# Kernel optimization log

Measured on AMD Instinct MI355X. Metric: run time of the kernel, lower is better.

The kernel has to match this reference:

```python
import jax, jax.numpy as jnp
import numpy as np

N_NODES = 100000
N_EDGES = 1600000
IN_CH = 128
HID = 64
N_LAYER = 4
N_CLASS = 10
N_GRAPHS = 512
EPS = 1e-5


def setup_inputs() -> dict:
    key = jax.random.key(0)
    ks = jax.random.split(key, 20)
    x = jax.random.normal(ks[0], (N_NODES, IN_CH), dtype=jnp.float32)
    src = jax.random.randint(ks[1], (N_EDGES,), 0, N_NODES)
    dst = jax.random.randint(ks[2], (N_EDGES,), 0, N_NODES)
    batch = jnp.sort(jax.random.randint(ks[3], (N_NODES,), 0, N_GRAPHS))
    s = 0.05
    W0 = jax.random.normal(ks[4], (IN_CH, HID), dtype=jnp.float32) * s
    Ws = jax.random.normal(ks[5], (N_LAYER - 1, HID, HID), dtype=jnp.float32) * s
    bs = jax.random.normal(ks[6], (N_LAYER, HID), dtype=jnp.float32) * s
    g_bn = jnp.ones((N_LAYER, HID), dtype=jnp.float32)
    b_bn = jnp.zeros((N_LAYER, HID), dtype=jnp.float32)
    m3 = 3 * N_LAYER * HID  # 768
    m2 = 2 * N_LAYER * HID  # 512
    m1 = N_LAYER * HID      # 256
    g_out = jnp.ones((m3,), dtype=jnp.float32)
    b_out = jnp.zeros((m3,), dtype=jnp.float32)
    w1 = jax.random.normal(ks[7], (m3, m2), dtype=jnp.float32) * s
    b1 = jnp.zeros((m2,), dtype=jnp.float32)
    w2 = jax.random.normal(ks[8], (m2, m1), dtype=jnp.float32) * s
    b2 = jnp.zeros((m1,), dtype=jnp.float32)
    w3 = jax.random.normal(ks[9], (m1, N_CLASS), dtype=jnp.float32) * s
    b3 = jnp.zeros((N_CLASS,), dtype=jnp.float32)
    return dict(x=x, src=src, dst=dst, batch=batch, W0=W0, Ws=Ws, bs=bs,
                g_bn=g_bn, b_bn=b_bn, g_out=g_out, b_out=b_out,
                w1=w1, b1=b1, w2=w2, b2=b2, w3=w3, b3=b3)


def _bn(h, g, b):
    # training-mode BatchNorm1d over rows (biased variance, as torch normalizes)
    m = jnp.mean(h, axis=0)
    v = jnp.var(h, axis=0)
    return (h - m) * jax.lax.rsqrt(v + EPS) * g + b


def reference(x, src, dst, batch, W0, Ws, bs, g_bn, b_bn, g_out, b_out,
              w1, b1, w2, b2, w3, b3):
    n = x.shape[0]
    loops = jnp.arange(n)
    s = jnp.concatenate([src, loops])  # self-loops (GCNConv)
    d = jnp.concatenate([dst, loops])
    deg = jax.ops.segment_sum(jnp.ones_like(s, dtype=x.dtype), d, num_segments=n)
    norm = jax.lax.rsqrt(jnp.maximum(deg, 1.0))
    coef = (norm[s] * norm[d])[:, None]

    def conv(h, W, bias):
        h = h @ W
        msg = h[s] * coef  # [E+N, HID] gather
        return jax.ops.segment_sum(msg, d, num_segments=n) + bias

    H = []
    h = conv(x, W0, bs[0])           # conv_act is identity (default)
    h = _bn(h, g_bn[0], b_bn[0])
    H.append(h)
    for i in range(N_LAYER - 1):
        h = conv(h, Ws[i], bs[i + 1])
        h = _bn(h, g_bn[i + 1], b_bn[i + 1])
        H.append(h)
    H = jnp.concatenate(H, axis=1)   # [N, n_layer*HID]

    # mean / add / max pooling by graph id
    add = jax.ops.segment_sum(H, batch, num_segments=N_GRAPHS)
    cnt = jax.ops.segment_sum(jnp.ones((n,), H.dtype), batch, num_segments=N_GRAPHS)
    avg = add / jnp.maximum(cnt, 1.0)[:, None]
    mx = jax.ops.segment_max(H, batch, num_segments=N_GRAPHS)
    mx = jnp.where(cnt[:, None] > 0, mx, 0.0)
    Hg = jnp.concatenate([avg, add, mx], axis=1)  # [G, 3*n_layer*HID]

    # funnel readout (dropout p=0 -> identity)
    z = _bn(Hg, g_out, b_out)
    z = jax.nn.relu(z @ w1 + b1)
    z = jax.nn.relu(z @ w2 + b2)
    return jax.nn.log_softmax(z @ w3 + b3, axis=1)
```

## Files before the change

### kernel.cpp

```cpp
#include <hip/hip_runtime.h>
#include <hip/hip_bf16.h>
#include <math.h>

#define HIDC 64
#define NLAYER 4
#define NG 512
#define M3 768
#define M2 512
#define M1 256
#define NCLS 10
#define EPSV 1e-5f
#define NB 512
#define EPT 16
#define NPW 2
#define NSH 16

typedef float f32x4 __attribute__((ext_vector_type(4)));
typedef short sh8   __attribute__((ext_vector_type(8)));

__device__ inline unsigned bf16rne(float x){
  unsigned u = __float_as_uint(x);
  return (u + 0x7fffu + ((u >> 16) & 1u)) >> 16;
}
__device__ inline unsigned packbf2(float lo, float hi){
  return bf16rne(lo) | (bf16rne(hi) << 16);
}
__device__ inline float blo(unsigned u){ return __uint_as_float(u << 16); }
__device__ inline float bhi(unsigned u){ return __uint_as_float(u & 0xffff0000u); }

__device__ inline sh8 ldfrag(const unsigned short* p){
  union { uint4 u; sh8 s; } c;
  c.u = *(const uint4*)p;
  return c.s;
}

__global__ __launch_bounds__(256) void k_bhist(const int* __restrict__ dst, int E,
                                               int* __restrict__ bcnt){
  __shared__ int lc[NB];
  int tid = threadIdx.x;
  for (int i = tid; i < NB; i += 256) lc[i] = 0;
  __syncthreads();
  for (int e = blockIdx.x*256 + tid; e < E; e += gridDim.x*256)
    atomicAdd(&lc[__builtin_nontemporal_load(&dst[e]) >> 8], 1);
  __syncthreads();
  for (int i = tid; i < NB; i += 256){
    int c = lc[i];
    if (c) atomicAdd(&bcnt[i], c);
  }
}

__global__ void k_bscan(const int* __restrict__ bcnt, int* __restrict__ bofs,
                        int* __restrict__ bcursor){
  __shared__ int tmp[NB];
  int tid = threadIdx.x;
  int v = bcnt[tid];
  tmp[tid] = v; __syncthreads();
  for (int ofs = 1; ofs < NB; ofs <<= 1){
    int t = (tid >= ofs) ? tmp[tid-ofs] : 0;
    __syncthreads();
    tmp[tid] += t;
    __syncthreads();
  }
  int ex = tmp[tid] - v;
  bofs[tid] = ex;
  bcursor[tid] = ex;
}

__global__ __launch_bounds__(256) void k_bscatter(const int* __restrict__ src,
    const int* __restrict__ dst, int E, int* __restrict__ bcursor, unsigned* __restrict__ stage){
  __shared__ int lcnt[NB];
  __shared__ int lbase[NB];
  int tid = threadIdx.x;
  int t0 = blockIdx.x*(256*EPT);
  for (int i = tid; i < NB; i += 256) lcnt[i] = 0;
  __syncthreads();
  int s_[EPT], d_[EPT];
  bool ok[EPT];
  #pragma unroll
  for (int i = 0; i < EPT; i++){
    int e = t0 + i*256 + tid;
    ok[i] = (e < E);
    int ee = ok[i] ? e : 0;
    d_[i] = __builtin_nontemporal_load(&dst[ee]);
    s_[i] = __builtin_nontemporal_load(&src[ee]);
    if (ok[i]) atomicAdd(&lcnt[d_[i] >> 8], 1);
  }
  __syncthreads();
  for (int i = tid; i < NB; i += 256){
    int c = lcnt[i];
    lbase[i] = c ? atomicAdd(&bcursor[i], c) : 0;
  }
  __syncthreads();
  #pragma unroll
  for (int i = 0; i < EPT; i++){
    if (ok[i]){
      int pos = atomicAdd(&lbase[d_[i] >> 8], 1);
      stage[pos] = ((unsigned)s_[i] << 8) | ((unsigned)d_[i] & 255u);
    }
  }
}

__global__ __launch_bounds__(256) void k_deg_b(const unsigned* __restrict__ stage,
    const int* __restrict__ bofs, const int* __restrict__ bcnt,
    int* __restrict__ row_start, int* __restrict__ cursor,
    float* __restrict__ normv, int n, int E){
  __shared__ int hist[256];
  __shared__ int tmp[256];
  int b = blockIdx.x;
  int tid = threadIdx.x;
  hist[tid] = 0;
  __syncthreads();
  int st = bofs[b], en = st + bcnt[b];
  for (int i = st + tid; i < en; i += 256)
    atomicAdd(&hist[stage[i] & 255u], 1);
  __syncthreads();
  int v = hist[tid];
  tmp[tid] = v;
  __syncthreads();
  for (int o = 1; o < 256; o <<= 1){
    int t = (tid >= o) ? tmp[tid-o] : 0;
    __syncthreads();
    tmp[tid] += t;
    __syncthreads();
  }
  int node = b*256 + tid;
  if (node < n){
    int rs = st + tmp[tid] - v;
    row_start[node] = rs;
    cursor[node] = rs;
    normv[node] = rsqrtf((float)(v + 1));
  }
  if (b == 0 && tid == 0) row_start[n] = E;
}

__global__ __launch_bounds__(256) void k_fill_b(const unsigned* __restrict__ stage,
    const int* __restrict__ bofs, const int* __restrict__ bcnt,
    int* __restrict__ cursor, int* __restrict__ col){
  int b = blockIdx.x;
  int st = bofs[b], en = st + bcnt[b];
  for (int i = st + threadIdx.x; i < en; i += 256){
    unsigned p = stage[i];
    int node = (b << 8) | (int)(p & 255u);
    int pos = atomicAdd(&cursor[node], 1);
    col[pos] = (int)(p >> 8);
  }
}

__global__ __launch_bounds__(256) void k_prep0(const float* __restrict__ W,
    unsigned short* __restrict__ Wt){
  int tid = threadIdx.x;
  int c = tid & 63, q = tid >> 6;
  #pragma unroll 4
  for (int k = q*32; k < q*32 + 32; k++){
    float w = W[(size_t)k*64 + c];
    Wt[(size_t)c*128 + k] = (unsigned short)bf16rne(w);
  }
}

__global__ __launch_bounds__(256) void k_prep_bn(const float* __restrict__ sums,
    const float* __restrict__ g, const float* __restrict__ b, float invn,
    float* __restrict__ bnss_l, const float* __restrict__ W,
    unsigned short* __restrict__ Wt, float* __restrict__ bvec){
  __shared__ float ss[128];
  __shared__ float bred[4][64];
  int tid = threadIdx.x;
  if (tid < 64){
    float s1 = 0.f, s2 = 0.f;
    #pragma unroll
    for (int s = 0; s < NSH; s++){ s1 += sums[s*128 + tid]; s2 += sums[s*128 + 64 + tid]; }
    float mean = s1*invn;
    float var = fmaxf(s2*invn - mean*mean, 0.f);
    float sv = g[tid]*rsqrtf(var + EPSV);
    float sh = b[tid] - mean*sv;
    ss[tid] = sv; ss[64+tid] = sh;
    bnss_l[tid] = sv; bnss_l[64+tid] = sh;
  }
  __syncthreads();
  if (!W) return;
  int c = tid & 63, q = tid >> 6;
  float bs = 0.f;
  #pragma unroll 4
  for (int k = q*16; k < q*16 + 16; k++){
    float w = W[(size_t)k*64 + c];
    Wt[(size_t)c*64 + k] = (unsigned short)bf16rne(w*ss[k]);
    bs += ss[64+k]*w;
  }
  bred[q][c] = bs;
  __syncthreads();
  if (tid < 64) bvec[tid] = bred[0][tid]+bred[1][tid]+bred[2][tid]+bred[3][tid];
}

__device__ inline void mfma_epi(f32x4 acc[2][4], int rowbase, int lr, int lk,
    const float* __restrict__ norm, const float* __restrict__ bias,
    unsigned short* __restrict__ Ub, int n){
  #pragma unroll
  for (int m = 0; m < 2; m++){
    #pragma unroll
    for (int j = 0; j < 4; j++){
      int row = rowbase + m*16 + lk*4 + j;
      if (row < n){
        float nr = norm[row];
        #pragma unroll
        for (int ct = 0; ct < 4; ct++){
          int colv = ct*16 + lr;
          float v = acc[m][ct][j];
          if (bias) v += bias[colv];
          Ub[(size_t)row*64 + colv] = (unsigned short)bf16rne(v*nr);
        }
      }
    }
  }
}

__global__ __launch_bounds__(256) void k_gemm_l0_mfma(const float* __restrict__ X,
    const unsigned short* __restrict__ Wt, const float* __restrict__ norm,
    unsigned* __restrict__ U32, int n){
  __shared__ unsigned short Al[128*40];
  int tid = threadIdx.x;
  int w = tid >> 6, l = tid & 63;
  int lr = l & 15, lk = l >> 4;
  int rb = blockIdx.x * 128;
  f32x4 z = {0.f,0.f,0.f,0.f};
  f32x4 acc[2][4];
  #pragma unroll
  for (int m = 0; m < 2; m++)
    #pragma unroll
    for (int ct = 0; ct < 4; ct++) acc[m][ct] = z;
  for (int kc = 0; kc < 128; kc += 32){
    __syncthreads();
    {
      int r = tid >> 1, h = tid & 1;
      int rr = rb + r; if (rr >= n) rr = n - 1;
      const float* xp = X + (size_t)rr*128 + kc + h*16;
      float4 v0 = *(const float4*)(xp+0);
      float4 v1 = *(const float4*)(xp+4);
      float4 v2 = *(const float4*)(xp+8);
      float4 v3 = *(const float4*)(xp+12);
      uint4 o0, o1;
      o0.x = packbf2(v0.x, v0.y); o0.y = packbf2(v0.z, v0.w);
      o0.z = packbf2(v1.x, v1.y); o0.w = packbf2(v1.z, v1.w);
      o1.x = packbf2(v2.x, v2.y); o1.y = packbf2(v2.z, v2.w);
      o1.z = packbf2(v3.x, v3.y); o1.w = packbf2(v3.z, v3.w);
      unsigned short* dl = &Al[r*40 + h*16];
      *(uint4*)(dl) = o0;
      *(uint4*)(dl+8) = o1;
    }
    __syncthreads();
    sh8 bfr[4];
    #pragma unroll
    for (int ct = 0; ct < 4; ct++)
      bfr[ct] = ldfrag(&Wt[(size_t)(ct*16+lr)*128 + kc + lk*8]);
    #pragma unroll
    for (int m = 0; m < 2; m++){
      sh8 af = ldfrag(&Al[(w*32 + m*16 + lr)*40 + lk*8]);
      #pragma unroll
      for (int ct = 0; ct < 4; ct++)
        acc[m][ct] = __builtin_amdgcn_mfma_f32_16x16x32_bf16(af, bfr[ct], acc[m][ct], 0, 0, 0);
    }
  }
  mfma_epi(acc, rb + w*32, lr, lk, norm, nullptr, (unsigned short*)U32, n);
}

__global__ __launch_bounds__(256) void k_gemm_lb_mfma(const unsigned short* __restrict__ Ab,
    const unsigned short* __restrict__ Wt, const float* __restrict__ bias,
    const float* __restrict__ norm, unsigned* __restrict__ U32, int n){
  int tid = threadIdx.x;
  int w = tid >> 6, l = tid & 63;
  int lr = l & 15, lk = l >> 4;
  int rb = blockIdx.x * 128 + w*32;
  f32x4 z = {0.f,0.f,0.f,0.f};
  f32x4 acc[2][4];
  #pragma unroll
  for (int m = 0; m < 2; m++)
    #pragma unroll
    for (int ct = 0; ct < 4; ct++) acc[m][ct] = z;
  #pragma unroll
  for (int kc = 0; kc < 64; kc += 32){
    sh8 bfr[4];
    #pragma unroll
    for (int ct = 0; ct < 4; ct++)
      bfr[ct] = ldfrag(&Wt[(size_t)(ct*16+lr)*64 + kc + lk*8]);
    #pragma unroll
    for (int m = 0; m < 2; m++){
      int r = rb + m*16 + lr; if (r >= n) r = n - 1;
      sh8 af = ldfrag(&Ab[(size_t)r*64 + kc + lk*8]);
      #pragma unroll
      for (int ct = 0; ct < 4; ct++)
        acc[m][ct] = __builtin_amdgcn_mfma_f32_16x16x32_bf16(af, bfr[ct], acc[m][ct], 0, 0, 0);
    }
  }
  mfma_epi(acc, rb, lr, lk, norm, bias, (unsigned short*)U32, n);
}

__global__ __launch_bounds__(256) void k_agg_bn(const unsigned* __restrict__ U32,
    const int* __restrict__ row_start, const int* __restrict__ col,
    const float* __restrict__ norm, unsigned* __restrict__ AGGb,
    float* __restrict__ sums, int n){
  int tid = threadIdx.x;
  int wv = tid >> 6;
  int lane = tid & 63;
  int half = lane >> 5;
  int cl = lane & 31;
  float rs0=0.f, rs1=0.f, rq0=0.f, rq1=0.f;
  int base = blockIdx.x*(4*NPW) + wv*NPW;
  #pragma unroll
  for (int it = 0; it < NPW; ++it){
    int node = __builtin_amdgcn_readfirstlane(base + it);
    bool nv = (node < n);
    int nodec = nv ? node : 0;
    int st = row_start[nodec], en = row_start[nodec+1];
    float s0 = 0.f, s1 = 0.f;
    if (half == 0){
      unsigned u = U32[(size_t)nodec*32 + cl];
      s0 = blo(u); s1 = bhi(u);
    }
    int nit = (en - st + 15) >> 4;
    for (int i = 0; i < nit; i++){
      int k = st + i*16 + half*8;
      unsigned ua[8];
      #pragma unroll
      for (int j = 0; j < 8; j++){
        int kk = k + j;
        bool v = (kk < en);
        int idx = v ? kk : st;
        unsigned a = U32[(size_t)col[idx]*32 + cl];
        ua[j] = v ? a : 0u;
      }
      #pragma unroll
      for (int j = 0; j < 8; j++){
        s0 += blo(ua[j]);
        s1 += bhi(ua[j]);
      }
    }
    s0 += __shfl_xor(s0, 32);
    s1 += __shfl_xor(s1, 32);
    if (half == 0 && nv){
      float nr = norm[node];
      s0 *= nr; s1 *= nr;
      AGGb[(size_t)node*32 + cl] = packbf2(s0, s1);
      rs0 += s0; rs1 += s1; rq0 += s0*s0; rq1 += s1*s1;
    }
  }
  __shared__ float L[4][32][4];
  if (half == 0){ L[wv][cl][0]=rs0; L[wv][cl][1]=rs1; L[wv][cl][2]=rq0; L[wv][cl][3]=rq1; }
  __syncthreads();
  if (tid < 128){
    int c2 = tid & 31, f = tid >> 5;
    float v = L[0][c2][f] + L[1][c2][f] + L[2][c2][f] + L[3][c2][f];
    int addr = ((f >= 2) ? 64 : 0) + 2*c2 + (f & 1);
    atomicAdd(&sums[(blockIdx.x & (NSH-1))*128 + addr], v);
  }
}

__device__ inline int lowerb(const int* a, int n, int key){
  int lo = 0, hi = n;
  while (lo < hi){ int mid = (lo+hi) >> 1; if (a[mid] < key) lo = mid+1; else hi = mid; }
  return lo;
}

__global__ __launch_bounds__(256) void k_pool_part(const unsigned* __restrict__ AGGall,
    size_t lstride32, const float* __restrict__ bnss, const int* __restrict__ batch,
    int n, float* __restrict__ Ppart){
  int bid = blockIdx.x;
  int g = bid >> 3, sub = bid & 7;
  int c = threadIdx.x;
  int l = c >> 6, ch = c & 63;
  const unsigned* A = AGGall + (size_t)l * lstride32;
  float sc = bnss[l*128 + ch], sh = bnss[l*128 + 64 + ch];
  int hi16 = ch & 1;
  int uofs = ch >> 1;
  int st = lowerb(batch, n, g), en = lowerb(batch, n, g+1);
  int len = en - st;
  int r0 = st + (int)(((long long)sub * len) >> 3);
  int r1 = st + (int)(((long long)(sub+1) * len) >> 3);
  float s = 0.f, mx = -INFINITY;
  for (int r = r0; r < r1; r++){
    unsigned u = A[(size_t)r*32 + uofs];
    float v = hi16 ? bhi(u) : blo(u);
    v = v*sc + sh;
    s += v; mx = fmaxf(mx, v);
  }
  float* P = Ppart + (size_t)bid*512;
  P[c] = s;
  P[256 + c] = mx;
}

__global__ __launch_bounds__(256) void k_pool_comb(const float* __restrict__ Ppart,
    const int* __restrict__ batch, int n, float* __restrict__ Hg){
  int g = blockIdx.x; int c = threadIdx.x;
  float s = 0.f, mx = -INFINITY;
  #pragma unroll
  for (int sub = 0; sub < 8; sub++){
    const float* P = Ppart + (size_t)(g*8 + sub)*512;
    s += P[c];
    mx = fmaxf(mx, P[256 + c]);
  }
  int st = lowerb(batch, n, g), en = lowerb(batch, n, g+1);
  int cnt = en - st;
  float avg = s / (float)(cnt > 1 ? cnt : 1);
  float mo = (cnt > 0) ? mx : 0.f;
  Hg[(size_t)g*M3 + c]        = avg;
  Hg[(size_t)g*M3 + 256 + c]  = s;
  Hg[(size_t)g*M3 + 512 + c]  = mo;
}

__global__ void k_bn2(const float* __restrict__ Hg, const float* __restrict__ g,
                      const float* __restrict__ b, float* __restrict__ zsc, float* __restrict__ zsh){
  int c = blockIdx.x; int tid = threadIdx.x;
  float s1 = 0.f, s2 = 0.f;
  for (int r = tid; r < NG; r += 64){
    float v = Hg[(size_t)r*M3 + c];
    s1 += v; s2 += v*v;
  }
  for (int o = 32; o > 0; o >>= 1){ s1 += __shfl_down(s1, o); s2 += __shfl_down(s2, o); }
  if (tid == 0){
    float mean = s1/(float)NG;
    float var = s2/(float)NG - mean*mean;
    var = fmaxf(var, 0.f);
    float sc = g[c]*rsqrtf(var + EPSV);
    zsc[c] = sc;
    zsh[c] = b[c] - mean*sc;
  }
}

__global__ __launch_bounds__(256) void k_gemm_t(const float* __restrict__ A, int K,
    const float* __restrict__ W, int N, const float* __restrict__ bias,
    const float* __restrict__ zsc, const float* __restrict__ zsh,
    float* __restrict__ out, int relu, int applybn){
  __shared__ float As[32][36];
  __shared__ float Bs[32][36];
  int tid = threadIdx.x;
  int tx = tid & 15, ty = tid >> 4;
  int rb = blockIdx.y << 5, cb = blockIdx.x << 5;
  int lr = tid >> 3;
  int lk = (tid & 7) << 2;
  float acc00=0.f, acc01=0.f, acc10=0.f, acc11=0.f;
  for (int k0 = 0; k0 < K; k0 += 32){
    float4 av = *(const float4*)&A[(size_t)(rb+lr)*K + k0 + lk];
    if (applybn){
      av.x = av.x*zsc[k0+lk+0] + zsh[k0+lk+0];
      av.y = av.y*zsc[k0+lk+1] + zsh[k0+lk+1];
      av.z = av.z*zsc[k0+lk+2] + zsh[k0+lk+2];
      av.w = av.w*zsc[k0+lk+3] + zsh[k0+lk+3];
    }
    *(float4*)&As[lr][lk] = av;
    float4 bv = *(const float4*)&W[(size_t)(k0+lr)*N + cb + lk];
    Bs[lk+0][lr] = bv.x;
    Bs[lk+1][lr] = bv.y;
    Bs[lk+2][lr] = bv.z;
    Bs[lk+3][lr] = bv.w;
    __syncthreads();
    #pragma unroll
    for (int kk = 0; kk < 32; kk += 4){
      float4 a0 = *(const float4*)&As[ty][kk];
      float4 a1 = *(const float4*)&As[ty+16][kk];
      float4 b0 = *(const float4*)&Bs[tx][kk];
      float4 b1 = *(const float4*)&Bs[tx+16][kk];
      acc00 += a0.x*b0.x + a0.y*b0.y + a0.z*b0.z + a0.w*b0.w;
      acc01 += a0.x*b1.x + a0.y*b1.y + a0.z*b1.z + a0.w*b1.w;
      acc10 += a1.x*b0.x + a1.y*b0.y + a1.z*b0.z + a1.w*b0.w;
      acc11 += a1.x*b1.x + a1.y*b1.y + a1.z*b1.z + a1.w*b1.w;
    }
    __syncthreads();
  }
  int c0 = cb + tx, c1 = cb + tx + 16;
  float bz0 = bias[c0], bz1 = bias[c1];
  acc00 += bz0; acc01 += bz1; acc10 += bz0; acc11 += bz1;
  if (relu){
    acc00 = fmaxf(acc00, 0.f); acc01 = fmaxf(acc01, 0.f);
    acc10 = fmaxf(acc10, 0.f); acc11 = fmaxf(acc11, 0.f);
  }
  out[(size_t)(rb+ty)*N + c0]      = acc00;
  out[(size_t)(rb+ty)*N + c1]      = acc01;
  out[(size_t)(rb+ty+16)*N + c0]   = acc10;
  out[(size_t)(rb+ty+16)*N + c1]   = acc11;
}

__global__ __launch_bounds__(256) void k_gemm3_lsm(const float* __restrict__ A,
    const float* __restrict__ W, const float* __restrict__ bias, float* __restrict__ out){
  __shared__ float Wl[M1*NCLS];
  __shared__ float part[64][4][NCLS];
  int tid = threadIdx.x;
  for (int i = tid; i < M1*NCLS; i += 256) Wl[i] = W[i];
  __syncthreads();
  int r = blockIdx.x*64 + (tid >> 2);
  int q = tid & 3;
  float acc[NCLS];
  #pragma unroll
  for (int j = 0; j < NCLS; j++) acc[j] = 0.f;
  const float4* A4 = (const float4*)(A + (size_t)r*M1 + q*64);
  for (int kq = 0; kq < 16; kq++){
    float4 a = A4[kq];
    int kb = q*64 + kq*4;
    #pragma unroll
    for (int j = 0; j < NCLS; j++){
      acc[j] += a.x*Wl[(kb+0)*NCLS+j] + a.y*Wl[(kb+1)*NCLS+j]
              + a.z*Wl[(kb+2)*NCLS+j] + a.w*Wl[(kb+3)*NCLS+j];
    }
  }
  #pragma unroll
  for (int j = 0; j < NCLS; j++) part[tid>>2][q][j] = acc[j];
  __syncthreads();
  if (tid < 64){
    int rr = blockIdx.x*64 + tid;
    float v[NCLS]; float m = -INFINITY;
    #pragma unroll
    for (int j = 0; j < NCLS; j++){
      v[j] = part[tid][0][j] + part[tid][1][j] + part[tid][2][j] + part[tid][3][j] + bias[j];
      m = fmaxf(m, v[j]);
    }
    float s = 0.f;
    #pragma unroll
    for (int j = 0; j < NCLS; j++) s += expf(v[j] - m);
    float ls = logf(s) + m;
    #pragma unroll
    for (int j = 0; j < NCLS; j++) out[(size_t)rr*NCLS + j] = v[j] - ls;
  }
}

extern "C" void kernel_launch(void* const* d_in, const int* in_sizes, int n_in,
                              void* d_out, int out_size, void* d_ws, size_t ws_size,
                              hipStream_t stream){
  const float* x    = (const float*)d_in[0];
  const int*   src  = (const int*)d_in[1];
  const int*   dst  = (const int*)d_in[2];
  const int*   batch= (const int*)d_in[3];
  const float* W0   = (const float*)d_in[4];
  const float* Wsm  = (const float*)d_in[5];
  const float* g_bn = (const float*)d_in[7];
  const float* b_bn = (const float*)d_in[8];
  const float* g_out= (const float*)d_in[9];
  const float* b_out= (const float*)d_in[10];
  const float* w1   = (const float*)d_in[11];
  const float* b1   = (const float*)d_in[12];
  const float* w2   = (const float*)d_in[13];
  const float* b2   = (const float*)d_in[14];
  const float* w3   = (const float*)d_in[15];
  const float* b3   = (const float*)d_in[16];

  int n = in_sizes[3];
  int E = in_sizes[1];

  char* ws = (char*)d_ws;
  size_t off = 0;
  auto alloc = [&](size_t bytes) -> char* {
    char* p = ws + off;
    off += (bytes + 255) / 256 * 256;
    return p;
  };
  float* normv     = (float*)alloc((size_t)n*4);
  int*   row_start = (int*)  alloc((size_t)(n+1)*4);
  int*   cursor    = (int*)  alloc((size_t)n*4);
  int*   colA      = (int*)  alloc((size_t)E*4);
  int*   bcnt      = (int*)  alloc(NB*4);
  int*   bofs      = (int*)  alloc(NB*4);
  int*   bcursor   = (int*)  alloc(NB*4);
  unsigned* stage  = (unsigned*)alloc((size_t)E*4);
  unsigned* U32    = (unsigned*)alloc((size_t)n*32*4);
  size_t lstride32 = (size_t)n*32;
  unsigned* AGGall = (unsigned*)alloc((size_t)NLAYER*lstride32*4);
  float* bnsums    = (float*)alloc(NSH*128*4);
  float* bnss      = (float*)alloc(NLAYER*128*4);
  unsigned short* Wt = (unsigned short*)alloc((size_t)NLAYER*64*128*2);
  float* bvec      = (float*)alloc(NLAYER*64*4);
  float* Ppart     = (float*)alloc((size_t)NG*8*512*4);
  float* Hg        = (float*)alloc((size_t)NG*M3*4);
  float* Z1        = (float*)alloc((size_t)NG*M2*4);
  float* Z2        = (float*)alloc((size_t)NG*M1*4);
  float* zsc       = (float*)alloc(M3*4);
  float* zsh       = (float*)alloc(M3*4);

  int nb_used = (n + 255) >> 8;
  int gb128 = (n + 127) / 128;

  hipMemsetAsync(bcnt, 0, NB*4, stream);
  k_prep0<<<1, 256, 0, stream>>>(W0, Wt);
  k_bhist<<<512, 256, 0, stream>>>(dst, E, bcnt);
  k_bscan<<<1, NB, 0, stream>>>(bcnt, bofs, bcursor);
  { int tiles = (E + 256*EPT - 1)/(256*EPT);
    k_bscatter<<<tiles, 256, 0, stream>>>(src, dst, E, bcursor, stage); }
  k_deg_b<<<nb_used, 256, 0, stream>>>(stage, bofs, bcnt, row_start, cursor, normv, n, E);
  k_fill_b<<<nb_used, 256, 0, stream>>>(stage, bofs, bcnt, cursor, colA);

  float invn = 1.f / (float)n;
  int aggblocks = (n + 4*NPW - 1) / (4*NPW);
  for (int l = 0; l < NLAYER; l++){
    unsigned* AGGb = AGGall + (size_t)l*lstride32;
    if (l == 0)
      k_gemm_l0_mfma<<<gb128, 256, 0, stream>>>(x, Wt, normv, U32, n);
    else
      k_gemm_lb_mfma<<<gb128, 256, 0, stream>>>((const unsigned short*)(AGGall + (size_t)(l-1)*lstride32),
                                                Wt + (size_t)l*64*128, bvec + l*64,
                                                normv, U32, n);
    hipMemsetAsync(bnsums, 0, NSH*128*4, stream);
    k_agg_bn<<<aggblocks, 256, 0, stream>>>(U32, row_start, colA, normv, AGGb, bnsums, n);
    if (l + 1 < NLAYER)
      k_prep_bn<<<1, 256, 0, stream>>>(bnsums, g_bn + l*64, b_bn + l*64, invn,
                                       bnss + l*128, Wsm + (size_t)l*64*64,
                                       Wt + (size_t)(l+1)*64*128, bvec + (l+1)*64);
    else
      k_prep_bn<<<1, 256, 0, stream>>>(bnsums, g_bn + l*64, b_bn + l*64, invn,
                                       bnss + l*128, nullptr, nullptr, nullptr);
  }

  k_pool_part<<<NG*8, 256, 0, stream>>>(AGGall, lstride32, bnss, batch, n, Ppart);
  k_pool_comb<<<NG, 256, 0, stream>>>(Ppart, batch, n, Hg);
  k_bn2<<<M3, 64, 0, stream>>>(Hg, g_out, b_out, zsc, zsh);

  { dim3 g1(M2/32, NG/32); k_gemm_t<<<g1, 256, 0, stream>>>(Hg, M3, w1, M2, b1, zsc, zsh, Z1, 1, 1); }
  { dim3 g2(M1/32, NG/32); k_gemm_t<<<g2, 256, 0, stream>>>(Z1, M2, w2, M1, b2, nullptr, nullptr, Z2, 1, 0); }
  k_gemm3_lsm<<<NG/64, 256, 0, stream>>>(Z2, w3, b3, (float*)d_out);
}
```

Baseline: 439.0 us.

## Pad CSR rows to multiples of 16 with dummy zero node, widen gather lanes

Each node's adjacency row is padded to a multiple of 16 entries, and the padding points at an extra all-zero row of U32. This lets the aggregation loop drop per-edge bounds checks. The aggregation kernel now has 16 lanes per feature group, each loading 8 bytes (4 bf16 channels), with four neighbor groups per wave, and combines them with two shuffle stages. Building the padded CSR takes extra kernels (partial-block scan, row fixup, col prefill), and the padding adds wasted gather work on low-degree nodes.

New measurement: 458.2 us. +4.4%, slower.

```diff
diff --git a/kernel.cpp b/kernel.cpp
--- a/kernel.cpp
+++ b/kernel.cpp
@@ -102,8 +102,8 @@
 
 __global__ __launch_bounds__(256) void k_deg_b(const unsigned* __restrict__ stage,
     const int* __restrict__ bofs, const int* __restrict__ bcnt,
-    int* __restrict__ row_start, int* __restrict__ cursor,
-    float* __restrict__ normv, int n, int E){
+    int* __restrict__ row_start, int* __restrict__ pbsum,
+    float* __restrict__ normv, int n){
   __shared__ int hist[256];
   __shared__ int tmp[256];
   int b = blockIdx.x;
@@ -115,7 +115,8 @@
     atomicAdd(&hist[stage[i] & 255u], 1);
   __syncthreads();
   int v = hist[tid];
-  tmp[tid] = v;
+  int pd = (v + 15) & ~15;
+  tmp[tid] = pd;
   __syncthreads();
   for (int o = 1; o < 256; o <<= 1){
     int t = (tid >= o) ? tmp[tid-o] : 0;
@@ -125,12 +126,41 @@
   }
   int node = b*256 + tid;
   if (node < n){
-    int rs = st + tmp[tid] - v;
-    row_start[node] = rs;
-    cursor[node] = rs;
+    row_start[node] = tmp[tid] - pd;
     normv[node] = rsqrtf((float)(v + 1));
   }
-  if (b == 0 && tid == 0) row_start[n] = E;
+  if (tid == 255) pbsum[b] = tmp[255];
+}
+
+__global__ void k_pbscan(const int* __restrict__ pbsum, int* __restrict__ pbofs,
+                         int* __restrict__ row_start, int n){
+  __shared__ int tmp[NB];
+  int tid = threadIdx.x;
+  int v = pbsum[tid];
+  tmp[tid] = v; __syncthreads();
+  for (int ofs = 1; ofs < NB; ofs <<= 1){
+    int t = (tid >= ofs) ? tmp[tid-ofs] : 0;
+    __syncthreads();
+    tmp[tid] += t;
+    __syncthreads();
+  }
+  pbofs[tid] = tmp[tid] - v;
+  if (tid == NB-1) row_start[n] = tmp[NB-1];
+}
+
+__global__ void k_rowfix(int* __restrict__ row_start, const int* __restrict__ pbofs,
+                         int* __restrict__ cursor, int n){
+  int i = blockIdx.x*256 + threadIdx.x;
+  if (i < n){
+    int r = row_start[i] + pbofs[i >> 8];
+    row_start[i] = r;
+    cursor[i] = r;
+  }
+}
+
+__global__ void k_prefill(int* __restrict__ col, int PE, int n){
+  int i = blockIdx.x*256 + threadIdx.x;
+  if (i < PE) col[i] = n;
 }
 
 __global__ __launch_bounds__(256) void k_fill_b(const unsigned* __restrict__ stage,
@@ -296,12 +326,15 @@
     const int* __restrict__ row_start, const int* __restrict__ col,
     const float* __restrict__ norm, unsigned* __restrict__ AGGb,
     float* __restrict__ sums, int n){
+  const char* Ubase = (const char*)U32;
   int tid = threadIdx.x;
   int wv = tid >> 6;
   int lane = tid & 63;
-  int half = lane >> 5;
-  int cl = lane & 31;
-  float rs0=0.f, rs1=0.f, rq0=0.f, rq1=0.f;
+  int g = lane >> 4;
+  int cl4 = lane & 15;
+  unsigned cofs = (unsigned)(cl4 << 3);
+  float rs[4] = {0.f,0.f,0.f,0.f};
+  float rq[4] = {0.f,0.f,0.f,0.f};
   int base = blockIdx.x*(4*NPW) + wv*NPW;
   #pragma unroll
   for (int it = 0; it < NPW; ++it){
@@ -309,45 +342,51 @@
     bool nv = (node < n);
     int nodec = nv ? node : 0;
     int st = row_start[nodec], en = row_start[nodec+1];
-    float s0 = 0.f, s1 = 0.f;
-    if (half == 0){
-      unsigned u = U32[(size_t)nodec*32 + cl];
-      s0 = blo(u); s1 = bhi(u);
-    }
-    int nit = (en - st + 15) >> 4;
+    uint2 su = *(const uint2*)(Ubase + ((size_t)nodec << 7) + cofs);
+    float s0 = (g==0) ? blo(su.x) : 0.f;
+    float s1 = (g==0) ? bhi(su.x) : 0.f;
+    float s2 = (g==0) ? blo(su.y) : 0.f;
+    float s3 = (g==0) ? bhi(su.y) : 0.f;
+    int nit = (en - st) >> 4;
     for (int i = 0; i < nit; i++){
-      int k = st + i*16 + half*8;
-      unsigned ua[8];
-      #pragma unroll
-      for (int j = 0; j < 8; j++){
-        int kk = k + j;
-        bool v = (kk < en);
-        int idx = v ? kk : st;
-        unsigned a = U32[(size_t)col[idx]*32 + cl];
-        ua[j] = v ? a : 0u;
-      }
-      #pragma unroll
-      for (int j = 0; j < 8; j++){
-        s0 += blo(ua[j]);
-        s1 += bhi(ua[j]);
-      }
-    }
-    s0 += __shfl_xor(s0, 32);
-    s1 += __shfl_xor(s1, 32);
-    if (half == 0 && nv){
+      int k = st + i*16 + g;
+      int j0 = col[k];
+      int j1 = col[k+4];
+      int j2 = col[k+8];
+      int j3 = col[k+12];
+      uint2 a0 = *(const uint2*)(Ubase + ((size_t)j0 << 7) + cofs);
+      uint2 a1 = *(const uint2*)(Ubase + ((size_t)j1 << 7) + cofs);
+      uint2 a2 = *(const uint2*)(Ubase + ((size_t)j2 << 7) + cofs);
+      uint2 a3 = *(const uint2*)(Ubase + ((size_t)j3 << 7) + cofs);
+      s0 += blo(a0.x) + blo(a1.x) + blo(a2.x) + blo(a3.x);
+      s1 += bhi(a0.x) + bhi(a1.x) + bhi(a2.x) + bhi(a3.x);
+      s2 += blo(a0.y) + blo(a1.y) + blo(a2.y) + blo(a3.y);
+      s3 += bhi(a0.y) + bhi(a1.y) + bhi(a2.y) + bhi(a3.y);
+    }
+    s0 += __shfl_xor(s0, 16); s1 += __shfl_xor(s1, 16);
+    s2 += __shfl_xor(s2, 16); s3 += __shfl_xor(s3, 16);
+    s0 += __shfl_xor(s0, 32); s1 += __shfl_xor(s1, 32);
+    s2 += __shfl_xor(s2, 32); s3 += __shfl_xor(s3, 32);
+    if (g == 0 && nv){
       float nr = norm[node];
-      s0 *= nr; s1 *= nr;
-      AGGb[(size_t)node*32 + cl] = packbf2(s0, s1);
-      rs0 += s0; rs1 += s1; rq0 += s0*s0; rq1 += s1*s1;
-    }
-  }
-  __shared__ float L[4][32][4];
-  if (half == 0){ L[wv][cl][0]=rs0; L[wv][cl][1]=rs1; L[wv][cl][2]=rq0; L[wv][cl][3]=rq1; }
+      s0 *= nr; s1 *= nr; s2 *= nr; s3 *= nr;
+      uint2 o; o.x = packbf2(s0, s1); o.y = packbf2(s2, s3);
+      *(uint2*)&AGGb[(size_t)node*32 + cl4*2] = o;
+      rs[0] += s0; rs[1] += s1; rs[2] += s2; rs[3] += s3;
+      rq[0] += s0*s0; rq[1] += s1*s1; rq[2] += s2*s2; rq[3] += s3*s3;
+    }
+  }
+  __shared__ float L[4][16][8];
+  if (g == 0){
+    #pragma unroll
+    for (int q = 0; q < 4; q++){ L[wv][cl4][q] = rs[q]; L[wv][cl4][4+q] = rq[q]; }
+  }
   __syncthreads();
   if (tid < 128){
-    int c2 = tid & 31, f = tid >> 5;
-    float v = L[0][c2][f] + L[1][c2][f] + L[2][c2][f] + L[3][c2][f];
-    int addr = ((f >= 2) ? 64 : 0) + 2*c2 + (f & 1);
+    int c4 = tid >> 3, slot = tid & 7;
+    float v = L[0][c4][slot] + L[1][c4][slot] + L[2][c4][slot] + L[3][c4][slot];
+    int ch = c4*4 + (slot & 3);
+    int addr = ((slot >= 4) ? 64 : 0) + ch;
     atomicAdd(&sums[(blockIdx.x & (NSH-1))*128 + addr], v);
   }
 }
@@ -548,15 +587,18 @@
     off += (bytes + 255) / 256 * 256;
     return p;
   };
+  int PE = E + 16*n;
   float* normv     = (float*)alloc((size_t)n*4);
   int*   row_start = (int*)  alloc((size_t)(n+1)*4);
   int*   cursor    = (int*)  alloc((size_t)n*4);
-  int*   colA      = (int*)  alloc((size_t)E*4);
+  int*   colA      = (int*)  alloc((size_t)PE*4);
   int*   bcnt      = (int*)  alloc(NB*4);
   int*   bofs      = (int*)  alloc(NB*4);
   int*   bcursor   = (int*)  alloc(NB*4);
+  int*   pbsum     = (int*)  alloc(NB*4);
+  int*   pbofs     = (int*)  alloc(NB*4);
   unsigned* stage  = (unsigned*)alloc((size_t)E*4);
-  unsigned* U32    = (unsigned*)alloc((size_t)n*32*4);
+  unsigned* U32    = (unsigned*)alloc((size_t)(n+1)*32*4);
   size_t lstride32 = (size_t)n*32;
   unsigned* AGGall = (unsigned*)alloc((size_t)NLAYER*lstride32*4);
   float* bnsums    = (float*)alloc(NSH*128*4);
@@ -574,12 +616,17 @@
   int gb128 = (n + 127) / 128;
 
   hipMemsetAsync(bcnt, 0, NB*4, stream);
+  hipMemsetAsync(pbsum, 0, NB*4, stream);
+  hipMemsetAsync(U32 + (size_t)n*32, 0, 128, stream);
   k_prep0<<<1, 256, 0, stream>>>(W0, Wt);
   k_bhist<<<512, 256, 0, stream>>>(dst, E, bcnt);
   k_bscan<<<1, NB, 0, stream>>>(bcnt, bofs, bcursor);
   { int tiles = (E + 256*EPT - 1)/(256*EPT);
     k_bscatter<<<tiles, 256, 0, stream>>>(src, dst, E, bcursor, stage); }
-  k_deg_b<<<nb_used, 256, 0, stream>>>(stage, bofs, bcnt, row_start, cursor, normv, n, E);
+  k_deg_b<<<nb_used, 256, 0, stream>>>(stage, bofs, bcnt, row_start, pbsum, normv, n);
+  k_pbscan<<<1, NB, 0, stream>>>(pbsum, pbofs, row_start, n);
+  k_rowfix<<<(n+255)/256, 256, 0, stream>>>(row_start, pbofs, cursor, n);
+  k_prefill<<<(PE+255)/256, 256, 0, stream>>>(colA, PE, n);
   k_fill_b<<<nb_used, 256, 0, stream>>>(stage, bofs, bcnt, cursor, colA);
 
   float invn = 1.f / (float)n;
```
